# Kernel tuning notes

Measured on AMD Instinct MI355X. Metric: run time of the kernel, lower is better.

The kernel has to match this reference:

```python
import jax, jax.numpy as jnp
import numpy as np

B, T, D, H = 2, 1024, 1024, 16
DH = D // H
_PAIRS = [(0, 1), (0, 2), (0, 3), (1, 2), (1, 3), (2, 3)]
_J6 = jnp.array([[0, 0, 0, 0, 0, 1],
                 [0, 0, 0, 0, -1, 0],
                 [0, 0, 0, 1, 0, 0],
                 [0, 0, 1, 0, 0, 0],
                 [0, -1, 0, 0, 0, 0],
                 [1, 0, 0, 0, 0, 0]], dtype=jnp.float32)


def exterior(p1, p2):
    # Plucker coordinates of the line through 4-vectors p1, p2, L2-normalized.
    parts = [p1[..., i] * p2[..., j] - p1[..., j] * p2[..., i] for i, j in _PAIRS]
    L = jnp.stack(parts, axis=-1)  # (..., 6)
    n = jnp.maximum(jnp.linalg.norm(L, axis=-1, keepdims=True), 1e-12)
    return L / n


def setup_inputs() -> dict:
    key = jax.random.key(0)
    ks = jax.random.split(key, 10)
    s = 0.02
    return {
        "x": jax.random.normal(ks[0], (B, T, D), jnp.float32),
        "Wqkv": jax.random.normal(ks[1], (3 * D, D), jnp.float32) * s,
        "bqkv": jnp.zeros((3 * D,), jnp.float32),
        "W1w": jax.random.normal(ks[2], (4 * H, D), jnp.float32) * s,
        "W2w": jax.random.normal(ks[3], (4 * H, D), jnp.float32) * s,
        "W1r": jax.random.normal(ks[4], (4 * H, D), jnp.float32) * s,
        "W2r": jax.random.normal(ks[5], (4 * H, D), jnp.float32) * s,
        "bias_scale": jnp.full((H,), 0.1, jnp.float32),
        "Wout": jax.random.normal(ks[6], (D, D), jnp.float32) * s,
        "bout": jnp.zeros((D,), jnp.float32),
    }


def reference(x, Wqkv, bqkv, W1w, W2w, W1r, W2r, bias_scale, Wout, bout):
    Bb, Tt, Dd = x.shape
    scale = DH ** (-0.5)
    qkv = (x @ Wqkv.T + bqkv).reshape(Bb, Tt, 3, H, DH)
    q = jnp.transpose(qkv[:, :, 0], (0, 2, 1, 3))  # (B,H,T,dh)
    k = jnp.transpose(qkv[:, :, 1], (0, 2, 1, 3))
    v = jnp.transpose(qkv[:, :, 2], (0, 2, 1, 3))
    std_logits = jnp.einsum('bhtd,bhsd->bhts', q, k) * scale

    x_prev = jnp.concatenate([jnp.zeros((Bb, 1, Dd), x.dtype), x[:, :-1]], axis=1)
    w1 = (x_prev @ W1w.T).reshape(Bb, Tt, H, 4)
    w2 = (x @ W2w.T).reshape(Bb, Tt, H, 4)
    write_lines = exterior(w1, w2)  # (B,T,H,6)
    r1 = (x @ W1r.T).reshape(Bb, Tt, H, 4)
    r2 = (x @ W2r.T).reshape(Bb, Tt, H, 4)
    read_lines = exterior(r1, r2)  # (B,T,H,6)

    Jw = jnp.einsum('bthi,ij->bhtj', write_lines, _J6)  # (B,H,T,6)
    rd = jnp.transpose(read_lines, (0, 2, 1, 3))        # (B,H,T,6)

    outer = Jw[..., :, None] * Jw[..., None, :]          # (B,H,T,6,6)
    M_causal = jnp.cumsum(outer, axis=2)                 # running Gram state
    rd_M = jnp.einsum('bhti,bhtij->bhtj', rd, M_causal)  # (B,H,T,6)
    bias_raw = jnp.einsum('bhti,bhsi->bhts', rd_M, Jw)   # (B,H,T,T)
    bias = jnp.abs(bias_raw) * bias_scale.reshape(1, H, 1, 1)

    logits = std_logits + bias
    mask = jnp.triu(jnp.ones((Tt, Tt), bool), 1)
    logits = jnp.where(mask, -jnp.inf, logits)
    attn = jax.nn.softmax(logits, axis=-1)
    out = jnp.einsum('bhts,bhsd->bthd', attn, v).reshape(Bb, Tt, Dd)
    return out @ Wout.T + bout
```

## Files before the change

### kernel.cpp

```cpp
#include <hip/hip_runtime.h>
#include <math.h>

#define B_ 2
#define T_ 1024
#define D_ 1024
#define H_ 16
#define NA_ 3328

typedef __attribute__((ext_vector_type(8))) short bf16x8;
typedef __attribute__((ext_vector_type(4))) float f32x4;

__device__ inline unsigned short f2bf(float x) {
  return (unsigned short)((__float_as_uint(x) + 0x8000u) >> 16);
}
__device__ inline unsigned bfpack(float lo, float hi) {
  unsigned a = __float_as_uint(hi) + 0x8000u;
  unsigned b = __float_as_uint(lo) + 0x8000u;
  return __builtin_amdgcn_perm(a, b, 0x07060302);
}
__device__ inline void hl_split(float x, unsigned short& h, unsigned short& l) {
  unsigned short hh = f2bf(x);
  float hf = __uint_as_float(((unsigned)hh) << 16);
  l = f2bf(x - hf);
  h = hh;
}

#define G_PRO()                                                                \
  const int tid = threadIdx.x;                                                 \
  const int w = tid >> 6, lane = tid & 63;                                     \
  const int lr = lane & 15, g = lane >> 4;                                     \
  const int wm = (w >> 1) * 32, wn = (w & 1) * 64;                             \
  const int row = tid >> 2, qc = tid & 3;

#define G_LOADA(d, s) {                                                        \
  d[0] = *(const float4*)(Ap + (s) * 32);                                      \
  d[1] = *(const float4*)(Ap + (s) * 32 + 4); }
#define G_LOADB(d, s) {                                                        \
  d[0] = *(const float4*)(Bp + (s) * 32);                                      \
  d[1] = *(const float4*)(Bp + (s) * 32 + 4); }
#define G_STORE(bi, a, b) {                                                    \
  unsigned char* SA_ = Smem + (bi) * 8192;                                     \
  *(uint4*)(SA_ + qc * 2048 + row * 16) =                                      \
      make_uint4(bfpack(a[0].x, a[0].y), bfpack(a[0].z, a[0].w),               \
                 bfpack(a[1].x, a[1].y), bfpack(a[1].z, a[1].w));              \
  unsigned char* SB_ = Smem + 16384 + (bi) * 8192;                             \
  *(uint4*)(SB_ + qc * 2048 + row * 16) =                                      \
      make_uint4(bfpack(b[0].x, b[0].y), bfpack(b[0].z, b[0].w),               \
                 bfpack(b[1].x, b[1].y), bfpack(b[1].z, b[1].w)); }
#define G_COMPUTE(bi) {                                                        \
  const unsigned char* SA_ = Smem + (bi) * 8192;                               \
  const unsigned char* SB_ = Smem + 16384 + (bi) * 8192;                       \
  bf16x8 af[2], bfr[4];                                                        \
  _Pragma("unroll") for (int i = 0; i < 2; ++i)                                \
    af[i] = *(const bf16x8*)(SA_ + g * 2048 + (wm + i * 16 + lr) * 16);        \
  _Pragma("unroll") for (int j = 0; j < 4; ++j)                                \
    bfr[j] = *(const bf16x8*)(SB_ + g * 2048 + (wn + j * 16 + lr) * 16);       \
  _Pragma("unroll") for (int i = 0; i < 2; ++i)                                \
  _Pragma("unroll") for (int j = 0; j < 4; ++j)                                \
    acc[i][j] = __builtin_amdgcn_mfma_f32_16x16x32_bf16(af[i], bfr[j],         \
                                                        acc[i][j], 0, 0, 0); }
#define G_MAIN()                                                               \
  f32x4 acc[2][4];                                                             \
  const f32x4 zf = {0.f, 0.f, 0.f, 0.f};                                       \
  _Pragma("unroll") for (int i = 0; i < 2; ++i)                                \
  _Pragma("unroll") for (int j = 0; j < 4; ++j) acc[i][j] = zf;                \
  float4 a0[2], b0[2], a1[2], b1[2];                                           \
  G_LOADA(a0, 0); G_LOADB(b0, 0);                                              \
  G_STORE(0, a0, b0);                                                          \
  G_LOADA(a1, 1); G_LOADB(b1, 1);                                              \
  __syncthreads();                                                             \
  _Pragma("unroll 1") for (int s = 0; s < 32; s += 2) {                        \
    G_COMPUTE(0);                                                              \
    G_STORE(1, a1, b1);                                                        \
    if (s + 2 < 32) { G_LOADA(a0, s + 2); G_LOADB(b0, s + 2); }                \
    __syncthreads();                                                           \
    G_COMPUTE(1);                                                              \
    if (s + 2 < 32) G_STORE(0, a0, b0);                                        \
    if (s + 3 < 32) { G_LOADA(a1, s + 3); G_LOADB(b1, s + 3); }                \
    __syncthreads();                                                           \
  }

__global__ __launch_bounds__(512) void gemm_qkv(
    const float* __restrict__ A, const float* __restrict__ Wqkv,
    const float* __restrict__ bqkv,
    const float* __restrict__ W1w, const float* __restrict__ W2w,
    const float* __restrict__ W1r, const float* __restrict__ W2r,
    float* __restrict__ C)
{
  __shared__ __align__(16) unsigned char Smem[32768];
  const int m0 = blockIdx.y * 128, n0 = blockIdx.x * 128;
  G_PRO();
  const float* Ap = A + (size_t)(m0 + row) * 1024 + qc * 8;
  const float* Bp;
  {
    const int cg = n0 + row;
    if (cg < 3072) Bp = Wqkv + (size_t)cg * 1024;
    else {
      const int r2 = cg - 3072;
      const float* Wm = (r2 < 64) ? W1w : (r2 < 128) ? W2w : (r2 < 192) ? W1r : W2r;
      Bp = Wm + (size_t)(r2 & 63) * 1024;
    }
    Bp += qc * 8;
  }
  G_MAIN();
#pragma unroll
  for (int i = 0; i < 2; ++i) {
    const int rbase = m0 + wm + i * 16 + 4 * g;
#pragma unroll
    for (int j = 0; j < 4; ++j) {
      const int col = n0 + wn + j * 16 + lr;
      const float bb = (col < 3072) ? bqkv[col] : 0.f;
#pragma unroll
      for (int r = 0; r < 4; ++r)
        C[(size_t)(rbase + r) * NA_ + col] = acc[i][j][r] + bb;
    }
  }
}

__global__ __launch_bounds__(512) void gemm_out(
    const float* __restrict__ A, const float* __restrict__ Bm,
    const float* __restrict__ bias, float* __restrict__ C)
{
  __shared__ __align__(16) unsigned char Smem[32768];
  const int m0 = blockIdx.y * 128, n0 = blockIdx.x * 128;
  G_PRO();
  const float* Ap = A + (size_t)(m0 + row) * 1024 + qc * 8;
  const float* Bp = Bm + (size_t)(n0 + row) * 1024 + qc * 8;
  G_MAIN();
#pragma unroll
  for (int i = 0; i < 2; ++i) {
    const int rbase = m0 + wm + i * 16 + 4 * g;
#pragma unroll
    for (int j = 0; j < 4; ++j) {
      const int col = n0 + wn + j * 16 + lr;
      const float bb = bias[col];
#pragma unroll
      for (int r = 0; r < 4; ++r)
        C[(size_t)(rbase + r) * 1024 + col] = acc[i][j][r] + bb;
    }
  }
}

__global__ __launch_bounds__(256) void scan_kernel(
    const float* __restrict__ qkvp,
    unsigned* __restrict__ Jwpk, unsigned* __restrict__ rdMpk)
{
  __shared__ float sc[256][41];
  const int tid = threadIdx.x;
  const int bh = blockIdx.x;
  const int b = bh >> 4, h = bh & 15;
  const int t0 = tid * 4;

  float L[36];
#pragma unroll
  for (int i = 0; i < 36; ++i) L[i] = 0.f;

  for (int tt = 0; tt < 4; ++tt) {
    const int t = t0 + tt;
    const size_t rowt = ((size_t)(b * T_) + t) * NA_;
    float4 p1w = make_float4(0.f, 0.f, 0.f, 0.f);
    if (t > 0) p1w = *(const float4*)(qkvp + rowt - NA_ + 3072 + h * 4);
    const float4 p2w = *(const float4*)(qkvp + rowt + 3136 + h * 4);
    const float L0 = p1w.x * p2w.y - p1w.y * p2w.x;
    const float L1 = p1w.x * p2w.z - p1w.z * p2w.x;
    const float L2 = p1w.x * p2w.w - p1w.w * p2w.x;
    const float L3 = p1w.y * p2w.z - p1w.z * p2w.y;
    const float L4 = p1w.y * p2w.w - p1w.w * p2w.y;
    const float L5 = p1w.z * p2w.w - p1w.w * p2w.z;
    const float n = sqrtf(L0 * L0 + L1 * L1 + L2 * L2 + L3 * L3 + L4 * L4 + L5 * L5);
    const float inv = 1.f / fmaxf(n, 1e-12f);
    const float jv[6] = {L5 * inv, -L4 * inv, L3 * inv, L2 * inv, -L1 * inv, L0 * inv};
    unsigned short JH[6], JL[6];
#pragma unroll
    for (int k = 0; k < 6; ++k) hl_split(jv[k], JH[k], JL[k]);
    unsigned* jp = Jwpk + (((size_t)bh * T_ + t) << 4);
    const unsigned h01 = JH[0] | ((unsigned)JH[1] << 16);
    const unsigned h23 = JH[2] | ((unsigned)JH[3] << 16);
    const unsigned h45 = JH[4] | ((unsigned)JH[5] << 16);
    jp[0] = h01; jp[1] = h23; jp[2] = h45;
    jp[3] = JL[0] | ((unsigned)JL[1] << 16);
    jp[4] = JL[2] | ((unsigned)JL[3] << 16);
    jp[5] = JL[4] | ((unsigned)JL[5] << 16);
    jp[6] = h01; jp[7] = h23; jp[8] = h45;
#pragma unroll
    for (int k = 9; k < 16; ++k) jp[k] = 0;
#pragma unroll
    for (int a = 0; a < 6; ++a)
#pragma unroll
      for (int c2 = 0; c2 < 6; ++c2)
        L[a * 6 + c2] = fmaf(jv[a], jv[c2], L[a * 6 + c2]);
  }

  float M[36];
#pragma unroll
  for (int i = 0; i < 36; ++i) M[i] = L[i];
#pragma unroll
  for (int k = 0; k < 9; ++k)
    *(float4*)&sc[tid][k * 4] = make_float4(M[k*4], M[k*4+1], M[k*4+2], M[k*4+3]);
  __syncthreads();
  for (int off = 1; off < 256; off <<= 1) {
    float4 tmp[9];
    const bool act = (tid >= off);
    if (act) {
#pragma unroll
      for (int k = 0; k < 9; ++k) tmp[k] = *(const float4*)&sc[tid - off][k * 4];
    }
    __syncthreads();
    if (act) {
#pragma unroll
      for (int k = 0; k < 9; ++k) {
        M[k*4]   += tmp[k].x; M[k*4+1] += tmp[k].y;
        M[k*4+2] += tmp[k].z; M[k*4+3] += tmp[k].w;
      }
#pragma unroll
      for (int k = 0; k < 9; ++k)
        *(float4*)&sc[tid][k * 4] = make_float4(M[k*4], M[k*4+1], M[k*4+2], M[k*4+3]);
    }
    __syncthreads();
  }

  float Mp[36];
#pragma unroll
  for (int i = 0; i < 36; ++i) Mp[i] = M[i] - L[i];

  for (int tt = 0; tt < 4; ++tt) {
    const int t = t0 + tt;
    const size_t rowt = ((size_t)(b * T_) + t) * NA_;
    float4 p1w = make_float4(0.f, 0.f, 0.f, 0.f);
    if (t > 0) p1w = *(const float4*)(qkvp + rowt - NA_ + 3072 + h * 4);
    const float4 p2w = *(const float4*)(qkvp + rowt + 3136 + h * 4);
    const float4 p1r = *(const float4*)(qkvp + rowt + 3200 + h * 4);
    const float4 p2r = *(const float4*)(qkvp + rowt + 3264 + h * 4);
    float jv[6], rv[6];
    {
      const float L0 = p1w.x * p2w.y - p1w.y * p2w.x;
      const float L1 = p1w.x * p2w.z - p1w.z * p2w.x;
      const float L2 = p1w.x * p2w.w - p1w.w * p2w.x;
      const float L3 = p1w.y * p2w.z - p1w.z * p2w.y;
      const float L4 = p1w.y * p2w.w - p1w.w * p2w.y;
      const float L5 = p1w.z * p2w.w - p1w.w * p2w.z;
      const float n = sqrtf(L0*L0 + L1*L1 + L2*L2 + L3*L3 + L4*L4 + L5*L5);
      const float inv = 1.f / fmaxf(n, 1e-12f);
      jv[0] = L5*inv; jv[1] = -L4*inv; jv[2] = L3*inv;
      jv[3] = L2*inv; jv[4] = -L1*inv; jv[5] = L0*inv;
    }
    {
      const float L0 = p1r.x * p2r.y - p1r.y * p2r.x;
      const float L1 = p1r.x * p2r.z - p1r.z * p2r.x;
      const float L2 = p1r.x * p2r.w - p1r.w * p2r.x;
      const float L3 = p1r.y * p2r.z - p1r.z * p2r.y;
      const float L4 = p1r.y * p2r.w - p1r.w * p2r.y;
      const float L5 = p1r.z * p2r.w - p1r.w * p2r.z;
      const float n = sqrtf(L0*L0 + L1*L1 + L2*L2 + L3*L3 + L4*L4 + L5*L5);
      const float inv = 1.f / fmaxf(n, 1e-12f);
      rv[0] = L0*inv; rv[1] = L1*inv; rv[2] = L2*inv;
      rv[3] = L3*inv; rv[4] = L4*inv; rv[5] = L5*inv;
    }
#pragma unroll
    for (int a = 0; a < 6; ++a)
#pragma unroll
      for (int c2 = 0; c2 < 6; ++c2)
        Mp[a * 6 + c2] = fmaf(jv[a], jv[c2], Mp[a * 6 + c2]);
    float s6[6];
#pragma unroll
    for (int jj = 0; jj < 6; ++jj) {
      float s = 0.f;
#pragma unroll
      for (int a = 0; a < 6; ++a) s = fmaf(rv[a], Mp[a * 6 + jj], s);
      s6[jj] = s;
    }
    unsigned short hh[6], ll[6];
#pragma unroll
    for (int i = 0; i < 6; ++i) hl_split(s6[i], hh[i], ll[i]);
    unsigned* ob = rdMpk + (((size_t)bh * T_ + t) << 4);
    const unsigned h01 = hh[0] | ((unsigned)hh[1] << 16);
    const unsigned h23 = hh[2] | ((unsigned)hh[3] << 16);
    const unsigned h45 = hh[4] | ((unsigned)hh[5] << 16);
    ob[0] = h01; ob[1] = h23; ob[2] = h45;
    ob[3] = h01; ob[4] = h23; ob[5] = h45;
    ob[6] = ll[0] | ((unsigned)ll[1] << 16);
    ob[7] = ll[2] | ((unsigned)ll[3] << 16);
    ob[8] = ll[4] | ((unsigned)ll[5] << 16);
#pragma unroll
    for (int i = 9; i < 16; ++i) ob[i] = 0;
  }
}

__global__ __launch_bounds__(256) void attn_mfma(
    const float* __restrict__ qkvp,
    const unsigned* __restrict__ Jwpk,
    const unsigned* __restrict__ rdMpk,
    const float* __restrict__ bias_scale,
    float* __restrict__ attnout)
{
  __shared__ __align__(16) unsigned char smem[40960];
  unsigned char* KT = smem;
  unsigned char* VT = smem + 16384;
  unsigned char* PB = smem + 32768;

  const int gid = blockIdx.x;
  const int bh = gid & 31;
  const int c = (gid < 256) ? (15 - (gid >> 5)) : ((gid - 256) >> 5);
  const int b = bh >> 4, h = bh & 15;
  const int tid = threadIdx.x;
  const int w = tid >> 6;
  const int lane = tid & 63;
  const int lr = lane & 15;
  const int g = lane >> 4;
  const int t0 = c * 64;
  const int nT = c + 1;

  const float* Rows = qkvp + (size_t)b * T_ * NA_ + h * 64;
  const size_t jb = (size_t)(b * H_ + h) * T_;

  bf16x8 qa[2];
  {
    const float* qp = Rows + (size_t)(t0 + w * 16 + lr) * NA_;
#pragma unroll
    for (int kb = 0; kb < 2; ++kb) {
      const float4 f0 = *(const float4*)(qp + kb * 32 + g * 8);
      const float4 f1 = *(const float4*)(qp + kb * 32 + g * 8 + 4);
      union { uint4 u; bf16x8 v; } qq;
      qq.u = make_uint4(bfpack(f0.x, f0.y), bfpack(f0.z, f0.w),
                        bfpack(f1.x, f1.y), bfpack(f1.z, f1.w));
      qa[kb] = qq.v;
    }
  }
  bf16x8 ra = *(const bf16x8*)(rdMpk + ((jb + t0 + w * 16 + lr) << 4) + g * 4);
  const float bsc = bias_scale[h];

  float m[4], lsum[4];
  f32x4 O[4];
  const f32x4 zf = {0.f, 0.f, 0.f, 0.f};
#pragma unroll
  for (int r = 0; r < 4; ++r) { m[r] = -1e30f; lsum[r] = 0.f; }
#pragma unroll
  for (int d = 0; d < 4; ++d) O[d] = zf;

  const int kr = tid >> 2, kc = tid & 3;
  const int sp = tid & 31, d8 = tid >> 5;

  float4 kA[4], vA0, vA1, vA2, vA3, kN[4], vN0, vN1, vN2, vN3;
  {
    const float* kp = Rows + (size_t)kr * NA_ + 1024 + kc * 16;
#pragma unroll
    for (int i = 0; i < 4; ++i) kA[i] = *(const float4*)(kp + i * 4);
    const float* vr = Rows + (size_t)(2 * sp) * NA_ + 2048 + d8 * 8;
    vA0 = *(const float4*)vr;         vA1 = *(const float4*)(vr + 4);
    vA2 = *(const float4*)(vr + NA_); vA3 = *(const float4*)(vr + NA_ + 4);
  }

  for (int ti = 0; ti < nT; ++ti) {
    const int s0 = ti * 64;
    const int buf = ti & 1;
    {
      unsigned char* kt = KT + buf * 8192;
      const float e[16] = {kA[0].x, kA[0].y, kA[0].z, kA[0].w,
                           kA[1].x, kA[1].y, kA[1].z, kA[1].w,
                           kA[2].x, kA[2].y, kA[2].z, kA[2].w,
                           kA[3].x, kA[3].y, kA[3].z, kA[3].w};
      const int swz = (kr & 7) << 4;
      uint4 w0, w1;
      w0.x = bfpack(e[0], e[1]);  w0.y = bfpack(e[2], e[3]);
      w0.z = bfpack(e[4], e[5]);  w0.w = bfpack(e[6], e[7]);
      w1.x = bfpack(e[8], e[9]);  w1.y = bfpack(e[10], e[11]);
      w1.z = bfpack(e[12], e[13]); w1.w = bfpack(e[14], e[15]);
      *(uint4*)(kt + kr * 128 + ((kc * 32) ^ swz))      = w0;
      *(uint4*)(kt + kr * 128 + ((kc * 32 + 16) ^ swz)) = w1;
    }
    {
      unsigned* vt = (unsigned*)(VT + buf * 8192);
      const float r0[8] = {vA0.x, vA0.y, vA0.z, vA0.w, vA1.x, vA1.y, vA1.z, vA1.w};
      const float r1[8] = {vA2.x, vA2.y, vA2.z, vA2.w, vA3.x, vA3.y, vA3.z, vA3.w};
#pragma unroll
      for (int i = 0; i < 8; ++i) {
        const int d = d8 * 8 + i;
        vt[d * 32 + (sp ^ ((d & 7) << 2))] = bfpack(r0[i], r1[i]);
      }
    }
    if (ti + 1 < nT) {
      const float* kp = Rows + (size_t)(s0 + 64 + kr) * NA_ + 1024 + kc * 16;
#pragma unroll
      for (int i = 0; i < 4; ++i) kN[i] = *(const float4*)(kp + i * 4);
      const float* vr = Rows + (size_t)(s0 + 64 + 2 * sp) * NA_ + 2048 + d8 * 8;
      vN0 = *(const float4*)vr;         vN1 = *(const float4*)(vr + 4);
      vN2 = *(const float4*)(vr + NA_); vN3 = *(const float4*)(vr + NA_ + 4);
    }
    asm volatile("s_waitcnt lgkmcnt(0)" ::: "memory");
    __builtin_amdgcn_sched_barrier(0);
    __builtin_amdgcn_s_barrier();
    __builtin_amdgcn_sched_barrier(0);

    f32x4 S[4], Sb[4];
    const unsigned char* kt = KT + buf * 8192;
    __builtin_amdgcn_s_setprio(1);
#pragma unroll
    for (int cb = 0; cb < 4; ++cb) {
      const int srw = cb * 16 + lr;
      f32x4 a = zf;
#pragma unroll
      for (int kb = 0; kb < 2; ++kb) {
        const bf16x8 kf = *(const bf16x8*)(kt + srw * 128 + (((kb * 64) + 16 * g) ^ ((srw & 7) << 4)));
        a = __builtin_amdgcn_mfma_f32_16x16x32_bf16(qa[kb], kf, a, 0, 0, 0);
      }
      S[cb] = a;
      const bf16x8 jw = *(const bf16x8*)(Jwpk + ((jb + s0 + cb * 16 + lr) << 4) + g * 4);
      Sb[cb] = __builtin_amdgcn_mfma_f32_16x16x32_bf16(ra, jw, zf, 0, 0, 0);
    }
    __builtin_amdgcn_s_setprio(0);

    const bool diag = (s0 == t0);
    float logit[4][4];
#pragma unroll
    for (int cb = 0; cb < 4; ++cb) {
#pragma unroll
      for (int r = 0; r < 4; ++r) {
        float lg = S[cb][r] * 0.125f + fabsf(Sb[cb][r]) * bsc;
        if (diag && (cb * 16 + lr > w * 16 + 4 * g + r)) lg = -1e30f;
        logit[cb][r] = lg;
      }
    }
    float mxr[4];
#pragma unroll
    for (int r = 0; r < 4; ++r) {
      float mx = fmaxf(fmaxf(logit[0][r], logit[1][r]), fmaxf(logit[2][r], logit[3][r]));
      mx = fmaxf(mx, __shfl_xor(mx, 1));
      mx = fmaxf(mx, __shfl_xor(mx, 2));
      mx = fmaxf(mx, __shfl_xor(mx, 4));
      mx = fmaxf(mx, __shfl_xor(mx, 8));
      mxr[r] = mx;
    }
    bool need = false;
#pragma unroll
    for (int r = 0; r < 4; ++r) need = need || (mxr[r] > m[r] + 8.f);
    if (__any(need)) {
#pragma unroll
      for (int r = 0; r < 4; ++r) {
        const float nm = fmaxf(m[r], mxr[r]);
        const float sc = __expf(m[r] - nm);
        m[r] = nm;
        lsum[r] *= sc;
#pragma unroll
        for (int d = 0; d < 4; ++d) O[d][r] *= sc;
      }
    }
#pragma unroll
    for (int cb = 0; cb < 4; ++cb) {
#pragma unroll
      for (int r = 0; r < 4; ++r) {
        const float p = __expf(logit[cb][r] - m[r]);
        lsum[r] += p;
        const int q = 4 * g + r;
        const int s = cb * 16 + lr;
        const int byte = w * 2048 + q * 128 + ((2 * s) ^ ((q & 7) << 4));
        *(unsigned short*)(PB + byte) = f2bf(p);
      }
    }
    asm volatile("s_waitcnt lgkmcnt(0)" ::: "memory");
    __builtin_amdgcn_sched_barrier(0);

    bf16x8 pa[2];
#pragma unroll
    for (int kb = 0; kb < 2; ++kb) {
      const int byte = w * 2048 + lr * 128 + (((kb * 64) + 16 * g) ^ ((lr & 7) << 4));
      pa[kb] = *(const bf16x8*)(PB + byte);
    }
    const unsigned char* vtb = VT + buf * 8192;
    __builtin_amdgcn_s_setprio(1);
#pragma unroll
    for (int db = 0; db < 4; ++db) {
      const int d = db * 16 + lr;
#pragma unroll
      for (int kb = 0; kb < 2; ++kb) {
        const int byte = d * 128 + (((kb * 64) + 16 * g) ^ ((d & 7) << 4));
        const bf16x8 vf = *(const bf16x8*)(vtb + byte);
        O[db] = __builtin_amdgcn_mfma_f32_16x16x32_bf16(pa[kb], vf, O[db], 0, 0, 0);
      }
    }
    __builtin_amdgcn_s_setprio(0);
#pragma unroll
    for (int i = 0; i < 4; ++i) kA[i] = kN[i];
    vA0 = vN0; vA1 = vN1; vA2 = vN2; vA3 = vN3;
  }

#pragma unroll
  for (int r = 0; r < 4; ++r) {
    float l = lsum[r];
    l += __shfl_xor(l, 1);
    l += __shfl_xor(l, 2);
    l += __shfl_xor(l, 4);
    l += __shfl_xor(l, 8);
    lsum[r] = 1.f / l;
  }
  {
    const int qb = w * 16 + 4 * g;
#pragma unroll
    for (int db = 0; db < 4; ++db) {
#pragma unroll
      for (int r = 0; r < 4; ++r) {
        const int t = t0 + qb + r;
        attnout[(size_t)(b * T_ + t) * 1024 + h * 64 + db * 16 + lr] = O[db][r] * lsum[r];
      }
    }
  }
}

extern "C" void kernel_launch(void* const* d_in, const int* in_sizes, int n_in,
                              void* d_out, int out_size, void* d_ws, size_t ws_size,
                              hipStream_t stream)
{
  (void)in_sizes; (void)n_in; (void)out_size; (void)ws_size;
  const float* x    = (const float*)d_in[0];
  const float* Wqkv = (const float*)d_in[1];
  const float* bqkv = (const float*)d_in[2];
  const float* W1w  = (const float*)d_in[3];
  const float* W2w  = (const float*)d_in[4];
  const float* W1r  = (const float*)d_in[5];
  const float* W2r  = (const float*)d_in[6];
  const float* bsc  = (const float*)d_in[7];
  const float* Wout = (const float*)d_in[8];
  const float* bout = (const float*)d_in[9];
  float* out = (float*)d_out;

  float*    qkvp    = (float*)d_ws;
  unsigned* Jwpk    = (unsigned*)(qkvp + (size_t)2048 * NA_);
  unsigned* rdMpk   = Jwpk + 524288;
  float*    attnout = (float*)(rdMpk + 524288);

  gemm_qkv<<<dim3(26, 16), 512, 0, stream>>>(
      x, Wqkv, bqkv, W1w, W2w, W1r, W2r, qkvp);
  scan_kernel<<<dim3(B_ * H_), 256, 0, stream>>>(qkvp, Jwpk, rdMpk);
  attn_mfma<<<dim3(B_ * H_ * (T_ / 64)), 256, 0, stream>>>(
      qkvp, Jwpk, rdMpk, bsc, attnout);
  gemm_out<<<dim3(8, 16), 512, 0, stream>>>(attnout, Wout, bout, out);
}
```

Before: 118.6 us.

## Split attention KV range across two warp groups with in-block softmax merge

```diff
diff --git a/kernel.cpp b/kernel.cpp
--- a/kernel.cpp
+++ b/kernel.cpp
@@ -286,29 +286,31 @@
   }
 }
 
-__global__ __launch_bounds__(256) void attn_mfma(
+__global__ __launch_bounds__(512) void attn_mfma(
     const float* __restrict__ qkvp,
     const unsigned* __restrict__ Jwpk,
     const unsigned* __restrict__ rdMpk,
     const float* __restrict__ bias_scale,
     float* __restrict__ attnout)
 {
-  __shared__ __align__(16) unsigned char smem[40960];
-  unsigned char* KT = smem;
-  unsigned char* VT = smem + 16384;
-  unsigned char* PB = smem + 32768;
+  __shared__ __align__(16) unsigned char smem[49152];
 
   const int gid = blockIdx.x;
   const int bh = gid & 31;
-  const int c = (gid < 256) ? (15 - (gid >> 5)) : ((gid - 256) >> 5);
+  const int c = gid >> 5;
   const int b = bh >> 4, h = bh & 15;
   const int tid = threadIdx.x;
-  const int w = tid >> 6;
-  const int lane = tid & 63;
+  const int grp = tid >> 8;
+  const int gtid = tid & 255;
+  const int w = gtid >> 6;
+  const int lane = gtid & 63;
   const int lr = lane & 15;
   const int g = lane >> 4;
   const int t0 = c * 64;
-  const int nT = c + 1;
+
+  unsigned char* KT = smem + grp * 24576;
+  unsigned char* VT = KT + 8192;
+  unsigned char* PB = KT + 16384;
 
   const float* Rows = qkvp + (size_t)b * T_ * NA_ + h * 64;
   const size_t jb = (size_t)(b * H_ + h) * T_;
@@ -337,48 +339,52 @@
 #pragma unroll
   for (int d = 0; d < 4; ++d) O[d] = zf;
 
-  const int kr = tid >> 2, kc = tid & 3;
-  const int sp = tid & 31, d8 = tid >> 5;
+  const int kr = gtid >> 2, kc = gtid & 3;
+  const int sp = gtid & 31, d8 = gtid >> 5;
 
   float4 kA[4], vA0, vA1, vA2, vA3, kN[4], vN0, vN1, vN2, vN3;
-  {
-    const float* kp = Rows + (size_t)kr * NA_ + 1024 + kc * 16;
+  if (grp * 8 <= c) {
+    const int s0p = grp * 8 * 64;
+    const float* kp = Rows + (size_t)(s0p + kr) * NA_ + 1024 + kc * 16;
 #pragma unroll
     for (int i = 0; i < 4; ++i) kA[i] = *(const float4*)(kp + i * 4);
-    const float* vr = Rows + (size_t)(2 * sp) * NA_ + 2048 + d8 * 8;
+    const float* vr = Rows + (size_t)(s0p + 2 * sp) * NA_ + 2048 + d8 * 8;
     vA0 = *(const float4*)vr;         vA1 = *(const float4*)(vr + 4);
     vA2 = *(const float4*)(vr + NA_); vA3 = *(const float4*)(vr + NA_ + 4);
   }
 
-  for (int ti = 0; ti < nT; ++ti) {
+  for (int it = 0; it < 8; ++it) {
+    const int ti = grp * 8 + it;
     const int s0 = ti * 64;
-    const int buf = ti & 1;
-    {
-      unsigned char* kt = KT + buf * 8192;
-      const float e[16] = {kA[0].x, kA[0].y, kA[0].z, kA[0].w,
-                           kA[1].x, kA[1].y, kA[1].z, kA[1].w,
-                           kA[2].x, kA[2].y, kA[2].z, kA[2].w,
-                           kA[3].x, kA[3].y, kA[3].z, kA[3].w};
-      const int swz = (kr & 7) << 4;
-      uint4 w0, w1;
-      w0.x = bfpack(e[0], e[1]);  w0.y = bfpack(e[2], e[3]);
-      w0.z = bfpack(e[4], e[5]);  w0.w = bfpack(e[6], e[7]);
-      w1.x = bfpack(e[8], e[9]);  w1.y = bfpack(e[10], e[11]);
-      w1.z = bfpack(e[12], e[13]); w1.w = bfpack(e[14], e[15]);
-      *(uint4*)(kt + kr * 128 + ((kc * 32) ^ swz))      = w0;
-      *(uint4*)(kt + kr * 128 + ((kc * 32 + 16) ^ swz)) = w1;
-    }
-    {
-      unsigned* vt = (unsigned*)(VT + buf * 8192);
-      const float r0[8] = {vA0.x, vA0.y, vA0.z, vA0.w, vA1.x, vA1.y, vA1.z, vA1.w};
-      const float r1[8] = {vA2.x, vA2.y, vA2.z, vA2.w, vA3.x, vA3.y, vA3.z, vA3.w};
-#pragma unroll
-      for (int i = 0; i < 8; ++i) {
-        const int d = d8 * 8 + i;
-        vt[d * 32 + (sp ^ ((d & 7) << 2))] = bfpack(r0[i], r1[i]);
-      }
-    }
-    if (ti + 1 < nT) {
+    const bool act = (ti <= c);
+    const bool pf = (it < 7) && (ti + 1 <= c);
+    if (act) {
+      {
+        const float e[16] = {kA[0].x, kA[0].y, kA[0].z, kA[0].w,
+                             kA[1].x, kA[1].y, kA[1].z, kA[1].w,
+                             kA[2].x, kA[2].y, kA[2].z, kA[2].w,
+                             kA[3].x, kA[3].y, kA[3].z, kA[3].w};
+        const int swz = (kr & 7) << 4;
+        uint4 w0, w1;
+        w0.x = bfpack(e[0], e[1]);  w0.y = bfpack(e[2], e[3]);
+        w0.z = bfpack(e[4], e[5]);  w0.w = bfpack(e[6], e[7]);
+        w1.x = bfpack(e[8], e[9]);  w1.y = bfpack(e[10], e[11]);
+        w1.z = bfpack(e[12], e[13]); w1.w = bfpack(e[14], e[15]);
+        *(uint4*)(KT + kr * 128 + ((kc * 32) ^ swz))      = w0;
+        *(uint4*)(KT + kr * 128 + ((kc * 32 + 16) ^ swz)) = w1;
+      }
+      {
+        unsigned* vt = (unsigned*)VT;
+        const float r0[8] = {vA0.x, vA0.y, vA0.z, vA0.w, vA1.x, vA1.y, vA1.z, vA1.w};
+        const float r1[8] = {vA2.x, vA2.y, vA2.z, vA2.w, vA3.x, vA3.y, vA3.z, vA3.w};
+#pragma unroll
+        for (int i = 0; i < 8; ++i) {
+          const int d = d8 * 8 + i;
+          vt[d * 32 + (sp ^ ((d & 7) << 2))] = bfpack(r0[i], r1[i]);
+        }
+      }
+    }
+    if (pf) {
       const float* kp = Rows + (size_t)(s0 + 64 + kr) * NA_ + 1024 + kc * 16;
 #pragma unroll
       for (int i = 0; i < 4; ++i) kN[i] = *(const float4*)(kp + i * 4);
@@ -391,98 +397,102 @@
     __builtin_amdgcn_s_barrier();
     __builtin_amdgcn_sched_barrier(0);
 
-    f32x4 S[4], Sb[4];
-    const unsigned char* kt = KT + buf * 8192;
-    __builtin_amdgcn_s_setprio(1);
-#pragma unroll
-    for (int cb = 0; cb < 4; ++cb) {
-      const int srw = cb * 16 + lr;
-      f32x4 a = zf;
+    if (act) {
+      f32x4 S[4], Sb[4];
+      __builtin_amdgcn_s_setprio(1);
+#pragma unroll
+      for (int cb = 0; cb < 4; ++cb) {
+        const int srw = cb * 16 + lr;
+        f32x4 a = zf;
+#pragma unroll
+        for (int kb = 0; kb < 2; ++kb) {
+          const bf16x8 kf = *(const bf16x8*)(KT + srw * 128 + (((kb * 64) + 16 * g) ^ ((srw & 7) << 4)));
+          a = __builtin_amdgcn_mfma_f32_16x16x32_bf16(qa[kb], kf, a, 0, 0, 0);
+        }
+        S[cb] = a;
+        const bf16x8 jw = *(const bf16x8*)(Jwpk + ((jb + s0 + cb * 16 + lr) << 4) + g * 4);
+        Sb[cb] = __builtin_amdgcn_mfma_f32_16x16x32_bf16(ra, jw, zf, 0, 0, 0);
+      }
+      __builtin_amdgcn_s_setprio(0);
+
+      const bool diag = (s0 == t0);
+      float logit[4][4];
+#pragma unroll
+      for (int cb = 0; cb < 4; ++cb) {
+#pragma unroll
+        for (int r = 0; r < 4; ++r) {
+          float lg = S[cb][r] * 0.125f + fabsf(Sb[cb][r]) * bsc;
+          if (diag && (cb * 16 + lr > w * 16 + 4 * g + r)) lg = -1e30f;
+          logit[cb][r] = lg;
+        }
+      }
+      float mxr[4];
+#pragma unroll
+      for (int r = 0; r < 4; ++r) {
+        float mx = fmaxf(fmaxf(logit[0][r], logit[1][r]), fmaxf(logit[2][r], logit[3][r]));
+        mx = fmaxf(mx, __shfl_xor(mx, 1));
+        mx = fmaxf(mx, __shfl_xor(mx, 2));
+        mx = fmaxf(mx, __shfl_xor(mx, 4));
+        mx = fmaxf(mx, __shfl_xor(mx, 8));
+        mxr[r] = mx;
+      }
+      bool need = false;
+#pragma unroll
+      for (int r = 0; r < 4; ++r) need = need || (mxr[r] > m[r] + 8.f);
+      if (__any(need)) {
+#pragma unroll
+        for (int r = 0; r < 4; ++r) {
+          const float nm = fmaxf(m[r], mxr[r]);
+          const float sc = __expf(m[r] - nm);
+          m[r] = nm;
+          lsum[r] *= sc;
+#pragma unroll
+          for (int d = 0; d < 4; ++d) O[d][r] *= sc;
+        }
+      }
+#pragma unroll
+      for (int cb = 0; cb < 4; ++cb) {
+#pragma unroll
+        for (int r = 0; r < 4; ++r) {
+          const float p = __expf(logit[cb][r] - m[r]);
+          lsum[r] += p;
+          const int q = 4 * g + r;
+          const int s = cb * 16 + lr;
+          const int byte = w * 2048 + q * 128 + ((2 * s) ^ ((q & 7) << 4));
+          *(unsigned short*)(PB + byte) = f2bf(p);
+        }
+      }
+      asm volatile("s_waitcnt lgkmcnt(0)" ::: "memory");
+      __builtin_amdgcn_sched_barrier(0);
+
+      bf16x8 pa[2];
 #pragma unroll
       for (int kb = 0; kb < 2; ++kb) {
-        const bf16x8 kf = *(const bf16x8*)(kt + srw * 128 + (((kb * 64) + 16 * g) ^ ((srw & 7) << 4)));
-        a = __builtin_amdgcn_mfma_f32_16x16x32_bf16(qa[kb], kf, a, 0, 0, 0);
-      }
-      S[cb] = a;
-      const bf16x8 jw = *(const bf16x8*)(Jwpk + ((jb + s0 + cb * 16 + lr) << 4) + g * 4);
-      Sb[cb] = __builtin_amdgcn_mfma_f32_16x16x32_bf16(ra, jw, zf, 0, 0, 0);
-    }
-    __builtin_amdgcn_s_setprio(0);
-
-    const bool diag = (s0 == t0);
-    float logit[4][4];
-#pragma unroll
-    for (int cb = 0; cb < 4; ++cb) {
-#pragma unroll
-      for (int r = 0; r < 4; ++r) {
-        float lg = S[cb][r] * 0.125f + fabsf(Sb[cb][r]) * bsc;
-        if (diag && (cb * 16 + lr > w * 16 + 4 * g + r)) lg = -1e30f;
-        logit[cb][r] = lg;
-      }
-    }
-    float mxr[4];
-#pragma unroll
-    for (int r = 0; r < 4; ++r) {
-      float mx = fmaxf(fmaxf(logit[0][r], logit[1][r]), fmaxf(logit[2][r], logit[3][r]));
-      mx = fmaxf(mx, __shfl_xor(mx, 1));
-      mx = fmaxf(mx, __shfl_xor(mx, 2));
-      mx = fmaxf(mx, __shfl_xor(mx, 4));
-      mx = fmaxf(mx, __shfl_xor(mx, 8));
-      mxr[r] = mx;
-    }
-    bool need = false;
-#pragma unroll
-    for (int r = 0; r < 4; ++r) need = need || (mxr[r] > m[r] + 8.f);
-    if (__any(need)) {
-#pragma unroll
-      for (int r = 0; r < 4; ++r) {
-        const float nm = fmaxf(m[r], mxr[r]);
-        const float sc = __expf(m[r] - nm);
-        m[r] = nm;
-        lsum[r] *= sc;
-#pragma unroll
-        for (int d = 0; d < 4; ++d) O[d][r] *= sc;
-      }
-    }
-#pragma unroll
-    for (int cb = 0; cb < 4; ++cb) {
-#pragma unroll
-      for (int r = 0; r < 4; ++r) {
-        const float p = __expf(logit[cb][r] - m[r]);
-        lsum[r] += p;
-        const int q = 4 * g + r;
-        const int s = cb * 16 + lr;
-        const int byte = w * 2048 + q * 128 + ((2 * s) ^ ((q & 7) << 4));
-        *(unsigned short*)(PB + byte) = f2bf(p);
-      }
-    }
-    asm volatile("s_waitcnt lgkmcnt(0)" ::: "memory");
-    __builtin_amdgcn_sched_barrier(0);
-
-    bf16x8 pa[2];
-#pragma unroll
-    for (int kb = 0; kb < 2; ++kb) {
-      const int byte = w * 2048 + lr * 128 + (((kb * 64) + 16 * g) ^ ((lr & 7) << 4));
-      pa[kb] = *(const bf16x8*)(PB + byte);
-    }
-    const unsigned char* vtb = VT + buf * 8192;
-    __builtin_amdgcn_s_setprio(1);
-#pragma unroll
-    for (int db = 0; db < 4; ++db) {
-      const int d = db * 16 + lr;
-#pragma unroll
-      for (int kb = 0; kb < 2; ++kb) {
-        const int byte = d * 128 + (((kb * 64) + 16 * g) ^ ((d & 7) << 4));
-        const bf16x8 vf = *(const bf16x8*)(vtb + byte);
-        O[db] = __builtin_amdgcn_mfma_f32_16x16x32_bf16(pa[kb], vf, O[db], 0, 0, 0);
-      }
-    }
-    __builtin_amdgcn_s_setprio(0);
-#pragma unroll
-    for (int i = 0; i < 4; ++i) kA[i] = kN[i];
-    vA0 = vN0; vA1 = vN1; vA2 = vN2; vA3 = vN3;
-  }
-
+        const int byte = w * 2048 + lr * 128 + (((kb * 64) + 16 * g) ^ ((lr & 7) << 4));
+        pa[kb] = *(const bf16x8*)(PB + byte);
+      }
+      __builtin_amdgcn_s_setprio(1);
+#pragma unroll
+      for (int db = 0; db < 4; ++db) {
+        const int d = db * 16 + lr;
+#pragma unroll
+        for (int kb = 0; kb < 2; ++kb) {
+          const int byte = d * 128 + (((kb * 64) + 16 * g) ^ ((d & 7) << 4));
+          const bf16x8 vf = *(const bf16x8*)(VT + byte);
+          O[db] = __builtin_amdgcn_mfma_f32_16x16x32_bf16(pa[kb], vf, O[db], 0, 0, 0);
+        }
+      }
+      __builtin_amdgcn_s_setprio(0);
+    }
+    __builtin_amdgcn_s_barrier();
+    if (pf) {
+#pragma unroll
+      for (int i = 0; i < 4; ++i) kA[i] = kN[i];
+      vA0 = vN0; vA1 = vN1; vA2 = vN2; vA3 = vN3;
+    }
+  }
+
+  float lrow[4];
 #pragma unroll
   for (int r = 0; r < 4; ++r) {
     float l = lsum[r];
@@ -490,16 +500,55 @@
     l += __shfl_xor(l, 2);
     l += __shfl_xor(l, 4);
     l += __shfl_xor(l, 8);
-    lsum[r] = 1.f / l;
-  }
-  {
-    const int qb = w * 16 + 4 * g;
-#pragma unroll
-    for (int db = 0; db < 4; ++db) {
+    lrow[r] = l;
+  }
+
+  float* OA = (float*)smem;
+  float* ML = (float*)(smem + 16384);
+  if (c >= 8 && grp == 0) {
+#pragma unroll
+    for (int db = 0; db < 4; ++db)
+#pragma unroll
+      for (int r = 0; r < 4; ++r)
+        OA[(w * 16 + 4 * g + r) * 64 + db * 16 + lr] = O[db][r];
+#pragma unroll
+    for (int r = 0; r < 4; ++r) {
+      ML[w * 16 + 4 * g + r] = m[r];
+      ML[64 + w * 16 + 4 * g + r] = lrow[r];
+    }
+  }
+  asm volatile("s_waitcnt lgkmcnt(0)" ::: "memory");
+  __builtin_amdgcn_sched_barrier(0);
+  __builtin_amdgcn_s_barrier();
+  __builtin_amdgcn_sched_barrier(0);
+
+  if (c >= 8) {
+    if (grp == 1) {
 #pragma unroll
       for (int r = 0; r < 4; ++r) {
-        const int t = t0 + qb + r;
-        attnout[(size_t)(b * T_ + t) * 1024 + h * 64 + db * 16 + lr] = O[db][r] * lsum[r];
+        const int q = w * 16 + 4 * g + r;
+        const float mA = ML[q], lA = ML[64 + q];
+        const float mst = fmaxf(mA, m[r]);
+        const float aA = __expf(mA - mst);
+        const float aB = __expf(m[r] - mst);
+        const float inv = 1.f / (lA * aA + lrow[r] * aB);
+        const int t = t0 + q;
+#pragma unroll
+        for (int db = 0; db < 4; ++db) {
+          const float v = (OA[q * 64 + db * 16 + lr] * aA + O[db][r] * aB) * inv;
+          attnout[(size_t)(b * T_ + t) * 1024 + h * 64 + db * 16 + lr] = v;
+        }
+      }
+    }
+  } else {
+    if (grp == 0) {
+#pragma unroll
+      for (int r = 0; r < 4; ++r) {
+        const float inv = 1.f / lrow[r];
+        const int t = t0 + w * 16 + 4 * g + r;
+#pragma unroll
+        for (int db = 0; db < 4; ++db)
+          attnout[(size_t)(b * T_ + t) * 1024 + h * 64 + db * 16 + lr] = O[db][r] * inv;
       }
     }
   }
@@ -530,7 +579,7 @@
   gemm_qkv<<<dim3(26, 16), 512, 0, stream>>>(
       x, Wqkv, bqkv, W1w, W2w, W1r, W2r, qkvp);
   scan_kernel<<<dim3(B_ * H_), 256, 0, stream>>>(qkvp, Jwpk, rdMpk);
-  attn_mfma<<<dim3(B_ * H_ * (T_ / 64)), 256, 0, stream>>>(
+  attn_mfma<<<dim3(B_ * H_ * (T_ / 64)), 512, 0, stream>>>(
       qkvp, Jwpk, rdMpk, bsc, attnout);
   gemm_out<<<dim3(8, 16), 512, 0, stream>>>(attnout, Wout, bout, out);
 }
```

After: 129.4 us. 9.1% more time.
